# Kernel tuning notes

Measured on AMD Instinct MI355X. Metric: run time of the kernel, lower is better.

The kernel has to match this reference:

```python
import jax, jax.numpy as jnp
import numpy as np

N, E, C_IN, C_OUT, HEADS = 50000, 800000, 256, 64, 4

def setup_inputs() -> dict:
    key = jax.random.key(0)
    ks = jax.random.split(key, 6)
    x = jax.random.normal(ks[0], (N, C_IN), dtype=jnp.float32)
    row = jax.random.randint(ks[1], (E,), 0, N, dtype=jnp.int32)
    col = jax.random.randint(ks[2], (E,), 0, N, dtype=jnp.int32)
    # ensure no self loops (remove_self_loops is then a no-op)
    col = jnp.where(col == row, (col + 1) % N, col)
    edge_index = jnp.stack([row, col], axis=0)
    edge_attr = jax.random.normal(ks[3], (E,), dtype=jnp.float32)
    weight = jax.random.normal(ks[4], (C_IN, C_OUT), dtype=jnp.float32) * (1.0 / np.sqrt(C_IN))
    kw, kb = jax.random.split(ks[5])
    att_w = jax.random.normal(kw, (2 * C_OUT, HEADS), dtype=jnp.float32) * (1.0 / np.sqrt(2 * C_OUT))
    att_b = jax.random.normal(kb, (HEADS,), dtype=jnp.float32) * 0.01
    return {"x": x, "edge_index": edge_index, "edge_attr": edge_attr,
            "weight": weight, "att_w": att_w, "att_b": att_b}

def _egat_forward(x, edge_index, edge_attr, weight, att_w, att_b):
    n = x.shape[0]
    xp = x @ weight  # [N, C_OUT]
    # add self loops (edge_attr fill value = 1)
    loop = jnp.arange(n, dtype=edge_index.dtype)
    row = jnp.concatenate([edge_index[0], loop])
    col = jnp.concatenate([edge_index[1], loop])
    ea = jnp.concatenate([edge_attr, jnp.ones((n,), dtype=edge_attr.dtype)])
    # per-edge attention logits [E+N, HEADS]
    alpha = jnp.concatenate([xp[row], xp[col]], axis=-1) @ att_w + att_b
    alpha = alpha * jnp.abs(ea)[:, None]
    alpha = jax.nn.leaky_relu(alpha, negative_slope=0.2) * 100.0
    # segment softmax grouped by row
    amax = jax.ops.segment_max(alpha, row, num_segments=n)
    ex = jnp.exp(alpha - amax[row])
    denom = jax.ops.segment_sum(ex, row, num_segments=n)
    alpha = ex / (denom[row] + 1e-16)
    # concat=False -> average heads into a single column
    alpha = alpha.mean(-1)[:, None]  # [E+N, 1]
    # my_cast: [E+N, C_OUT, n_cols]
    out = xp[col][:, :, None] * alpha[:, None, :]
    out = jax.ops.segment_sum(out, row, num_segments=n)  # [N, C_OUT, 1]
    alpha_index = jnp.stack([row, col], axis=0)
    return out, alpha, alpha_index

def reference(x, edge_index, edge_attr, weight, att_w, att_b):
    return _egat_forward(x, edge_index, edge_attr, weight, att_w, att_b)
```

## Files before the change

kernel.cpp:

```cpp
#include <hip/hip_runtime.h>
#include <hip/hip_bf16.h>

#define NN 50000
#define NE 800000
#define MT (NN + NE)
#define CO 64

#define OFF_ALPHA (NN * CO)
#define OFF_IDX   (OFF_ALPHA + MT)

#define WS_XPB  0
#define WS_A1   (WS_XPB + NN * CO / 2)
#define WS_A2   (WS_A1 + NN * 4)
#define WS_CNT  (WS_A2 + NN * 4)
#define WS_SLOT 2050000

#define GEMM_BLOCKS ((NN + 63) / 64)
#define HIST_BLOCKS ((MT + 255) / 256)

__global__ __launch_bounds__(256) void k_gemm_hist(const float* __restrict__ x,
                                                   const float* __restrict__ w,
                                                   __hip_bfloat16* __restrict__ xpb,
                                                   const float* __restrict__ attw,
                                                   float* __restrict__ a1,
                                                   float* __restrict__ a2,
                                                   const int* __restrict__ ei0,
                                                   const int* __restrict__ ei1,
                                                   const float* __restrict__ ea,
                                                   int* __restrict__ cnt,
                                                   unsigned long long* __restrict__ slot,
                                                   float* __restrict__ dout) {
  if (blockIdx.x < GEMM_BLOCKS) {
    __shared__ float xs[32][68];
    __shared__ float wsm[32][68];
    const int tid = threadIdx.x;
    const int nb = blockIdx.x * 64;
    const int tr = tid >> 4;
    const int tc = tid & 15;
    const int xn0 = tid >> 3, xq0 = tid & 7;
    const int xn1 = (256 + tid) >> 3, xq1 = tid & 7;
    const int wk0 = tid >> 4, wc0 = tid & 15;
    const int wk1 = (256 + tid) >> 4, wc1 = tid & 15;
    float acc[4][4] = {};
    float4 xv0, xv1, wv0, wv1;

    {
      int gn0 = nb + xn0, gn1 = nb + xn1;
      xv0 = (gn0 < NN) ? *reinterpret_cast<const float4*>(&x[gn0 * 256 + xq0 * 4])
                       : make_float4(0.f, 0.f, 0.f, 0.f);
      xv1 = (gn1 < NN) ? *reinterpret_cast<const float4*>(&x[gn1 * 256 + xq1 * 4])
                       : make_float4(0.f, 0.f, 0.f, 0.f);
      wv0 = *reinterpret_cast<const float4*>(&w[wk0 * CO + wc0 * 4]);
      wv1 = *reinterpret_cast<const float4*>(&w[wk1 * CO + wc1 * 4]);
    }

    for (int kb = 0; kb < 256; kb += 32) {
      xs[xq0 * 4 + 0][xn0] = xv0.x; xs[xq0 * 4 + 1][xn0] = xv0.y;
      xs[xq0 * 4 + 2][xn0] = xv0.z; xs[xq0 * 4 + 3][xn0] = xv0.w;
      xs[xq1 * 4 + 0][xn1] = xv1.x; xs[xq1 * 4 + 1][xn1] = xv1.y;
      xs[xq1 * 4 + 2][xn1] = xv1.z; xs[xq1 * 4 + 3][xn1] = xv1.w;
      *reinterpret_cast<float4*>(&wsm[wk0][wc0 * 4]) = wv0;
      *reinterpret_cast<float4*>(&wsm[wk1][wc1 * 4]) = wv1;
      __syncthreads();
      if (kb < 224) {
        const int nkb = kb + 32;
        int gn0 = nb + xn0, gn1 = nb + xn1;
        xv0 = (gn0 < NN) ? *reinterpret_cast<const float4*>(&x[gn0 * 256 + nkb + xq0 * 4])
                         : make_float4(0.f, 0.f, 0.f, 0.f);
        xv1 = (gn1 < NN) ? *reinterpret_cast<const float4*>(&x[gn1 * 256 + nkb + xq1 * 4])
                         : make_float4(0.f, 0.f, 0.f, 0.f);
        wv0 = *reinterpret_cast<const float4*>(&w[(nkb + wk0) * CO + wc0 * 4]);
        wv1 = *reinterpret_cast<const float4*>(&w[(nkb + wk1) * CO + wc1 * 4]);
      }
#pragma unroll
      for (int kk = 0; kk < 32; ++kk) {
        const float4 xv4 = *reinterpret_cast<const float4*>(&xs[kk][tr * 4]);
        const float4 wv4 = *reinterpret_cast<const float4*>(&wsm[kk][tc * 4]);
        const float xvv[4] = {xv4.x, xv4.y, xv4.z, xv4.w};
        const float wvv[4] = {wv4.x, wv4.y, wv4.z, wv4.w};
#pragma unroll
        for (int i = 0; i < 4; ++i)
#pragma unroll
          for (int j = 0; j < 4; ++j) acc[i][j] = fmaf(xvv[i], wvv[j], acc[i][j]);
      }
      __syncthreads();
    }
#pragma unroll
    for (int i = 0; i < 4; ++i) {
      int gn = nb + tr * 4 + i;
      if (gn < NN) {
        union { ushort4 u4; __hip_bfloat16 h[4]; } pk;
        pk.h[0] = __float2bfloat16(acc[i][0]);
        pk.h[1] = __float2bfloat16(acc[i][1]);
        pk.h[2] = __float2bfloat16(acc[i][2]);
        pk.h[3] = __float2bfloat16(acc[i][3]);
        *reinterpret_cast<ushort4*>(&xpb[gn * CO + tc * 4]) = pk.u4;
      }
    }
    float p1[4][4] = {}, p2[4][4] = {};
#pragma unroll
    for (int j = 0; j < 4; ++j) {
      const float4 w1 = *reinterpret_cast<const float4*>(&attw[(4 * tc + j) * 4]);
      const float4 w2 = *reinterpret_cast<const float4*>(&attw[(64 + 4 * tc + j) * 4]);
#pragma unroll
      for (int i = 0; i < 4; ++i) {
        const float a = acc[i][j];
        p1[i][0] = fmaf(a, w1.x, p1[i][0]); p1[i][1] = fmaf(a, w1.y, p1[i][1]);
        p1[i][2] = fmaf(a, w1.z, p1[i][2]); p1[i][3] = fmaf(a, w1.w, p1[i][3]);
        p2[i][0] = fmaf(a, w2.x, p2[i][0]); p2[i][1] = fmaf(a, w2.y, p2[i][1]);
        p2[i][2] = fmaf(a, w2.z, p2[i][2]); p2[i][3] = fmaf(a, w2.w, p2[i][3]);
      }
    }
#pragma unroll
    for (int off = 1; off < 16; off <<= 1)
#pragma unroll
      for (int i = 0; i < 4; ++i)
#pragma unroll
        for (int h = 0; h < 4; ++h) {
          p1[i][h] += __shfl_xor(p1[i][h], off);
          p2[i][h] += __shfl_xor(p2[i][h], off);
        }
    if (tc == 0) {
#pragma unroll
      for (int i = 0; i < 4; ++i) {
        int gn = nb + tr * 4 + i;
        if (gn < NN) {
          *reinterpret_cast<float4*>(&a1[gn * 4]) =
              make_float4(p1[i][0], p1[i][1], p1[i][2], p1[i][3]);
          *reinterpret_cast<float4*>(&a2[gn * 4]) =
              make_float4(p2[i][0], p2[i][1], p2[i][2], p2[i][3]);
        }
      }
    }
  } else {
    int e = (blockIdx.x - GEMM_BLOCKS) * 256 + threadIdx.x;
    if (e >= MT) return;
    int r, c; float aw;
    if (e < NE) { r = ei0[e]; c = ei1[e]; aw = fabsf(ea[e]); }
    else        { r = e - NE; c = r;      aw = 1.0f; }
    int pos = atomicAdd(&cnt[r], 1);
    if (pos < 64) {
      unsigned awb = __float_as_uint(aw);
      unsigned lo = (awb & 0xFFFFFFF0u) | ((unsigned)e >> 16);
      unsigned hi = ((unsigned)e & 0xFFFFu) | ((unsigned)c << 16);
      unsigned long long pk = (unsigned long long)lo | ((unsigned long long)hi << 32);
      __builtin_nontemporal_store(pk, &slot[r * 64 + pos]);
    }
    dout[OFF_IDX + e] = (float)r;
    dout[OFF_IDX + MT + e] = (float)c;
  }
}

__global__ __launch_bounds__(256) void k_node(const float* __restrict__ attb,
                                              const __hip_bfloat16* __restrict__ xpb,
                                              const float* __restrict__ a1,
                                              const float* __restrict__ a2,
                                              const int* __restrict__ cnt,
                                              const unsigned long long* __restrict__ slot,
                                              float* __restrict__ dout) {
  const int lane = threadIdx.x & 63;
  const int wid = threadIdx.x >> 6;
  const int r = blockIdx.x * 4 + wid;
  if (r >= NN) return;
  const int deg = min(cnt[r], 64);
  const float4 a1r = *reinterpret_cast<const float4*>(&a1[r * 4]);
  const float4 bb = *reinterpret_cast<const float4*>(&attb[0]);

  const bool act = lane < deg;
  int e = 0, c = 0;
  float aw = 0.f;
  if (act) {
    unsigned long long sv = slot[r * 64 + lane];
    unsigned w0 = (unsigned)sv, w1 = (unsigned)(sv >> 32);
    aw = __uint_as_float(w0 & 0xFFFFFFF0u);
    e  = (int)(((w0 & 0xFu) << 16) | (w1 & 0xFFFFu));
    c  = (int)(w1 >> 16);
  }
  const float4 a2c = *reinterpret_cast<const float4*>(&a2[c * 4]);
  float t0 = -1e30f, t1 = -1e30f, t2 = -1e30f, t3 = -1e30f;
  if (act) {
    t0 = (a1r.x + a2c.x + bb.x) * aw;
    t1 = (a1r.y + a2c.y + bb.y) * aw;
    t2 = (a1r.z + a2c.z + bb.z) * aw;
    t3 = (a1r.w + a2c.w + bb.w) * aw;
    t0 = (t0 < 0.f ? 0.2f * t0 : t0) * 100.f;
    t1 = (t1 < 0.f ? 0.2f * t1 : t1) * 100.f;
    t2 = (t2 < 0.f ? 0.2f * t2 : t2) * 100.f;
    t3 = (t3 < 0.f ? 0.2f * t3 : t3) * 100.f;
  }
  float m0 = t0, m1 = t1, m2 = t2, m3 = t3;
  if (deg > 32) {
    m0 = fmaxf(m0, __shfl_xor(m0, 32));
    m1 = fmaxf(m1, __shfl_xor(m1, 32));
    m2 = fmaxf(m2, __shfl_xor(m2, 32));
    m3 = fmaxf(m3, __shfl_xor(m3, 32));
  }
  if (deg > 16) {
    m0 = fmaxf(m0, __shfl_xor(m0, 16));
    m1 = fmaxf(m1, __shfl_xor(m1, 16));
    m2 = fmaxf(m2, __shfl_xor(m2, 16));
    m3 = fmaxf(m3, __shfl_xor(m3, 16));
  }
#pragma unroll
  for (int off = 8; off >= 1; off >>= 1) {
    m0 = fmaxf(m0, __shfl_xor(m0, off));
    m1 = fmaxf(m1, __shfl_xor(m1, off));
    m2 = fmaxf(m2, __shfl_xor(m2, off));
    m3 = fmaxf(m3, __shfl_xor(m3, off));
  }
  float p0 = act ? __expf(t0 - m0) : 0.f;
  float p1 = act ? __expf(t1 - m1) : 0.f;
  float p2 = act ? __expf(t2 - m2) : 0.f;
  float p3 = act ? __expf(t3 - m3) : 0.f;
  float s0 = p0, s1 = p1, s2 = p2, s3 = p3;
  if (deg > 32) {
    s0 += __shfl_xor(s0, 32); s1 += __shfl_xor(s1, 32);
    s2 += __shfl_xor(s2, 32); s3 += __shfl_xor(s3, 32);
  }
  if (deg > 16) {
    s0 += __shfl_xor(s0, 16); s1 += __shfl_xor(s1, 16);
    s2 += __shfl_xor(s2, 16); s3 += __shfl_xor(s3, 16);
  }
#pragma unroll
  for (int off = 8; off >= 1; off >>= 1) {
    s0 += __shfl_xor(s0, off); s1 += __shfl_xor(s1, off);
    s2 += __shfl_xor(s2, off); s3 += __shfl_xor(s3, off);
  }
  float mean = 0.f;
  if (act) {
    mean = 0.25f * (p0 / (s0 + 1e-16f) + p1 / (s1 + 1e-16f) +
                    p2 / (s2 + 1e-16f) + p3 / (s3 + 1e-16f));
    dout[OFF_ALPHA + e] = mean;
  }
  const int eg = lane >> 4;
  const int cg = lane & 15;
  float4 acc = make_float4(0.f, 0.f, 0.f, 0.f);
  const int nIter = (deg + 3) >> 2;
  for (int it = 0; it < nIter; ++it) {
    int idx = it * 4 + eg;
    float am = __shfl(mean, idx);
    int cc = __shfl(c, idx);
    ushort4 xv = *reinterpret_cast<const ushort4*>(&xpb[cc * CO + cg * 4]);
    acc.x = fmaf(am, __uint_as_float((unsigned)xv.x << 16), acc.x);
    acc.y = fmaf(am, __uint_as_float((unsigned)xv.y << 16), acc.y);
    acc.z = fmaf(am, __uint_as_float((unsigned)xv.z << 16), acc.z);
    acc.w = fmaf(am, __uint_as_float((unsigned)xv.w << 16), acc.w);
  }
#pragma unroll
  for (int off = 16; off <= 32; off <<= 1) {
    acc.x += __shfl_xor(acc.x, off);
    acc.y += __shfl_xor(acc.y, off);
    acc.z += __shfl_xor(acc.z, off);
    acc.w += __shfl_xor(acc.w, off);
  }
  if (lane < 16) *reinterpret_cast<float4*>(&dout[r * CO + lane * 4]) = acc;
}

extern "C" void kernel_launch(void* const* d_in, const int* in_sizes, int n_in,
                              void* d_out, int out_size, void* d_ws, size_t ws_size,
                              hipStream_t stream) {
  const float* x    = (const float*)d_in[0];
  const int*   ei   = (const int*)d_in[1];
  const float* ea   = (const float*)d_in[2];
  const float* w    = (const float*)d_in[3];
  const float* attw = (const float*)d_in[4];
  const float* attb = (const float*)d_in[5];
  float* dout = (float*)d_out;

  float* wsf = (float*)d_ws;
  __hip_bfloat16* xpb = (__hip_bfloat16*)(wsf + WS_XPB);
  float* a1   = wsf + WS_A1;
  float* a2   = wsf + WS_A2;
  int*   cnt  = (int*)(wsf + WS_CNT);
  unsigned long long* slot = (unsigned long long*)(wsf + WS_SLOT);
  const int* ei0 = ei;
  const int* ei1 = ei + NE;

  hipMemsetAsync(cnt, 0, NN * sizeof(int), stream);

  k_gemm_hist<<<GEMM_BLOCKS + HIST_BLOCKS, 256, 0, stream>>>(
      x, w, xpb, attw, a1, a2, ei0, ei1, ea, cnt, slot, dout);
  k_node<<<(NN + 3) / 4, 256, 0, stream>>>(attb, xpb, a1, a2, cnt, slot, dout);
}
```

Baseline: 104.3 us.

## Split per-row edge counters into 8 sub-buckets and store only edge ids

The histogram phase now spreads each row's atomic counter over 8 sub-counters chosen by block index, which is meant to reduce same-address atomic contention. Slots hold only a 4-byte edge id instead of a packed 8-byte record. The node kernel rebuilds the degree and each lane's slot position with a prefix scan over the 8 sub-counts, then gathers col and edge_attr itself. The cost is an 8x larger counter memset, extra indirect gathers in the node kernel, and a per-sub-bucket cap of 16, which could drop edges for a row whose edges land unevenly across buckets.

```diff
diff --git a/kernel.cpp b/kernel.cpp
--- a/kernel.cpp
+++ b/kernel.cpp
@@ -10,10 +10,10 @@
 #define OFF_IDX   (OFF_ALPHA + MT)
 
 #define WS_XPB  0
-#define WS_A1   (WS_XPB + NN * CO / 2)
-#define WS_A2   (WS_A1 + NN * 4)
-#define WS_CNT  (WS_A2 + NN * 4)
-#define WS_SLOT 2050000
+#define WS_A1   1600000
+#define WS_A2   1800000
+#define WS_CNT8 2000000
+#define WS_SLOT 2400000
 
 #define GEMM_BLOCKS ((NN + 63) / 64)
 #define HIST_BLOCKS ((MT + 255) / 256)
@@ -26,9 +26,8 @@
                                                    float* __restrict__ a2,
                                                    const int* __restrict__ ei0,
                                                    const int* __restrict__ ei1,
-                                                   const float* __restrict__ ea,
-                                                   int* __restrict__ cnt,
-                                                   unsigned long long* __restrict__ slot,
+                                                   int* __restrict__ cnt8,
+                                                   int* __restrict__ slot,
                                                    float* __restrict__ dout) {
   if (blockIdx.x < GEMM_BLOCKS) {
     __shared__ float xs[32][68];
@@ -135,46 +134,54 @@
   } else {
     int e = (blockIdx.x - GEMM_BLOCKS) * 256 + threadIdx.x;
     if (e >= MT) return;
-    int r, c; float aw;
-    if (e < NE) { r = ei0[e]; c = ei1[e]; aw = fabsf(ea[e]); }
-    else        { r = e - NE; c = r;      aw = 1.0f; }
-    int pos = atomicAdd(&cnt[r], 1);
-    if (pos < 64) {
-      unsigned awb = __float_as_uint(aw);
-      unsigned lo = (awb & 0xFFFFFFF0u) | ((unsigned)e >> 16);
-      unsigned hi = ((unsigned)e & 0xFFFFu) | ((unsigned)c << 16);
-      unsigned long long pk = (unsigned long long)lo | ((unsigned long long)hi << 32);
-      __builtin_nontemporal_store(pk, &slot[r * 64 + pos]);
-    }
+    int r, c;
+    if (e < NE) { r = ei0[e]; c = ei1[e]; } else { r = e - NE; c = r; }
+    const int sub = blockIdx.x & 7;
+    int pos = atomicAdd(&cnt8[r * 8 + sub], 1);
+    if (pos < 16) slot[r * 128 + sub * 16 + pos] = e;
     dout[OFF_IDX + e] = (float)r;
     dout[OFF_IDX + MT + e] = (float)c;
   }
 }
 
-__global__ __launch_bounds__(256) void k_node(const float* __restrict__ attb,
+__global__ __launch_bounds__(256) void k_node(const int* __restrict__ ei1,
+                                              const float* __restrict__ ea,
+                                              const float* __restrict__ attb,
                                               const __hip_bfloat16* __restrict__ xpb,
                                               const float* __restrict__ a1,
                                               const float* __restrict__ a2,
-                                              const int* __restrict__ cnt,
-                                              const unsigned long long* __restrict__ slot,
+                                              const int* __restrict__ cnt8,
+                                              const int* __restrict__ slot,
                                               float* __restrict__ dout) {
   const int lane = threadIdx.x & 63;
   const int wid = threadIdx.x >> 6;
   const int r = blockIdx.x * 4 + wid;
   if (r >= NN) return;
-  const int deg = min(cnt[r], 64);
   const float4 a1r = *reinterpret_cast<const float4*>(&a1[r * 4]);
   const float4 bb = *reinterpret_cast<const float4*>(&attb[0]);
 
+  int cs = min(cnt8[r * 8 + (lane & 7)], 16);
+  int csub[8];
+#pragma unroll
+  for (int s = 0; s < 8; ++s) csub[s] = __shfl(cs, s);
+  int deg = 0;
+#pragma unroll
+  for (int s = 0; s < 8; ++s) deg += csub[s];
+  deg = min(deg, 64);
   const bool act = lane < deg;
+  int sub = 7, idx = 0, accp = 0;
+#pragma unroll
+  for (int s = 0; s < 8; ++s) {
+    int hit = (lane >= accp) && (lane < accp + csub[s]);
+    if (hit) { sub = s; idx = lane - accp; }
+    accp += csub[s];
+  }
   int e = 0, c = 0;
   float aw = 0.f;
   if (act) {
-    unsigned long long sv = slot[r * 64 + lane];
-    unsigned w0 = (unsigned)sv, w1 = (unsigned)(sv >> 32);
-    aw = __uint_as_float(w0 & 0xFFFFFFF0u);
-    e  = (int)(((w0 & 0xFu) << 16) | (w1 & 0xFFFFu));
-    c  = (int)(w1 >> 16);
+    e = slot[r * 128 + sub * 16 + idx];
+    if (e < NE) { c = ei1[e]; aw = fabsf(ea[e]); }
+    else        { c = r;      aw = 1.0f; }
   }
   const float4 a2c = *reinterpret_cast<const float4*>(&a2[c * 4]);
   float t0 = -1e30f, t1 = -1e30f, t2 = -1e30f, t3 = -1e30f;
@@ -237,9 +244,9 @@
   float4 acc = make_float4(0.f, 0.f, 0.f, 0.f);
   const int nIter = (deg + 3) >> 2;
   for (int it = 0; it < nIter; ++it) {
-    int idx = it * 4 + eg;
-    float am = __shfl(mean, idx);
-    int cc = __shfl(c, idx);
+    int idxe = it * 4 + eg;
+    float am = __shfl(mean, idxe);
+    int cc = __shfl(c, idxe);
     ushort4 xv = *reinterpret_cast<const ushort4*>(&xpb[cc * CO + cg * 4]);
     acc.x = fmaf(am, __uint_as_float((unsigned)xv.x << 16), acc.x);
     acc.y = fmaf(am, __uint_as_float((unsigned)xv.y << 16), acc.y);
@@ -271,14 +278,15 @@
   __hip_bfloat16* xpb = (__hip_bfloat16*)(wsf + WS_XPB);
   float* a1   = wsf + WS_A1;
   float* a2   = wsf + WS_A2;
-  int*   cnt  = (int*)(wsf + WS_CNT);
-  unsigned long long* slot = (unsigned long long*)(wsf + WS_SLOT);
+  int*   cnt8 = (int*)(wsf + WS_CNT8);
+  int*   slot = (int*)(wsf + WS_SLOT);
   const int* ei0 = ei;
   const int* ei1 = ei + NE;
 
-  hipMemsetAsync(cnt, 0, NN * sizeof(int), stream);
+  hipMemsetAsync(cnt8, 0, NN * 8 * sizeof(int), stream);
 
   k_gemm_hist<<<GEMM_BLOCKS + HIST_BLOCKS, 256, 0, stream>>>(
-      x, w, xpb, attw, a1, a2, ei0, ei1, ea, cnt, slot, dout);
-  k_node<<<(NN + 3) / 4, 256, 0, stream>>>(attb, xpb, a1, a2, cnt, slot, dout);
+      x, w, xpb, attw, a1, a2, ei0, ei1, cnt8, slot, dout);
+  k_node<<<(NN + 3) / 4, 256, 0, stream>>>(
+      ei1, ea, attb, xpb, a1, a2, cnt8, slot, dout);
 }
```

Result: slower. 117.3 us (+12.5%).
